# Performance work log

Measured on AMD Instinct MI355X. Metric: run time of the kernel, lower is better.

The kernel has to match this reference:

```python
import math
import jax, jax.numpy as jnp
import numpy as np

D_MODEL = 1024
N_HEADS = 16
D_K = D_MODEL // N_HEADS


def _build_neighbours(n_heads):
    # Mirrors LatticeMultiHeadAttention._build_neighbours for a (4,4)-style lattice.
    side = int(math.sqrt(n_heads))
    cols = side + 1 if side * side < n_heads else side
    positions = [divmod(i, cols) for i in range(n_heads)]
    pos_map = {p: j for j, p in enumerate(positions)}
    nb_idx = np.full((n_heads, 8), -1, dtype=np.int64)
    nb_w = np.zeros((n_heads, 8), dtype=np.float32)
    for i, (r, c) in enumerate(positions):
        k = 0
        for dr in (-1, 0, 1):
            for dc in (-1, 0, 1):
                if dr == 0 and dc == 0:
                    continue
                j = pos_map.get((r + dr, c + dc))
                if j is not None and k < 8:
                    nb_idx[i, k] = j
                    nb_w[i, k] = math.exp(-math.hypot(dr, dc))
                    k += 1
    return nb_idx, nb_w


def _phase_biases(coupling):
    # Sequential Kuramoto phase update: head h uses neighbor phases already
    # updated for heads < h (exactly as the torch per-head loop mutates buffers).
    H = coupling.shape[0]
    nb_idx, nb_w = _build_neighbours(H)
    phases = [jnp.asarray(0.0, coupling.dtype) for _ in range(H)]
    two_pi = 2.0 * math.pi
    for h in range(H):
        force = jnp.asarray(0.0, coupling.dtype)
        for k in range(8):
            j = int(nb_idx[h, k])
            if j >= 0:
                force = force + jnp.asarray(nb_w[h, k], coupling.dtype) * jnp.sin(phases[j] - phases[h])
        intrinsic = 1.0 + 0.1 * h
        new_phase = (phases[h] + 0.01 * (intrinsic + coupling[h] * force)) % two_pi
        phases[h] = new_phase
    return 0.1 * jnp.cos(jnp.stack(phases))  # [H] per-head scalar bias


def setup_inputs() -> dict:
    key = jax.random.key(0)
    ks = jax.random.split(key, 9)
    B, L = 2, 2048
    std = 0.02
    return {
        "query": jax.random.normal(ks[0], (B, L, D_MODEL), jnp.float32),
        "key": jax.random.normal(ks[1], (B, L, D_MODEL), jnp.float32),
        "value": jax.random.normal(ks[2], (B, L, D_MODEL), jnp.float32),
        "Wq": std * jax.random.normal(ks[3], (N_HEADS, D_MODEL, D_K), jnp.float32),
        "Wk": std * jax.random.normal(ks[4], (N_HEADS, D_MODEL, D_K), jnp.float32),
        "Wv": std * jax.random.normal(ks[5], (N_HEADS, D_MODEL, D_K), jnp.float32),
        "out_w": std * jax.random.normal(ks[6], (D_MODEL, D_MODEL), jnp.float32),
        "out_b": jnp.zeros((D_MODEL,), jnp.float32),
        "coupling": 0.1 * jnp.ones((N_HEADS,), jnp.float32),
    }


def reference(query, key, value, Wq, Wk, Wv, out_w, out_b, coupling):
    d_k = Wq.shape[-1]
    Q = jnp.einsum("bld,hdk->bhlk", query, Wq)
    K = jnp.einsum("bld,hdk->bhlk", key, Wk)
    V = jnp.einsum("bld,hdk->bhlk", value, Wv)
    scale = jnp.asarray(math.sqrt(float(d_k)), query.dtype)
    scores = jnp.einsum("bhlk,bhmk->bhlm", Q, K) / scale
    bias = _phase_biases(coupling)  # [H]
    scores = scores + bias[None, :, None, None]
    attn = jax.nn.softmax(scores, axis=-1)
    ctx = jnp.einsum("bhlm,bhmk->bhlk", attn, V)
    B, H, L, _ = ctx.shape
    out = ctx.transpose(0, 2, 1, 3).reshape(B, L, H * d_k)  # concat heads
    return out @ out_w + out_b
```

## Files before the change

### kernel.cpp

```cpp
#include <hip/hip_runtime.h>
#include <cstdint>

typedef uint16_t u16;
typedef __attribute__((ext_vector_type(8))) short bf16x8;
typedef __attribute__((ext_vector_type(4))) short bf16x4;
typedef __attribute__((ext_vector_type(4))) float f32x4;

#define QSCALE 0.18033688011112042f

struct Ptr3 { const float* a; const float* b; const float* c; };

__device__ __forceinline__ u16 f2bf(float x) {
  union { float f; uint32_t u; } v; v.f = x;
  uint32_t r = (v.u + 0x7fffu + ((v.u >> 16) & 1u)) >> 16;
  return (u16)r;
}

__device__ __forceinline__ void async16(void* lds, const void* g) {
  __builtin_amdgcn_global_load_lds((const __attribute__((address_space(1))) void*)g,
                                   (__attribute__((address_space(3))) void*)lds, 16, 0, 0);
}

__global__ __launch_bounds__(256) void k_cast3(Ptr3 in, u16* __restrict__ out) {
  const int z = blockIdx.y;
  const float* p = z == 0 ? in.a : (z == 1 ? in.b : in.c);
  int i = blockIdx.x * 256 + threadIdx.x;
  float4 v = ((const float4*)p)[i];
  bf16x4 o;
  o[0] = (short)f2bf(v.x); o[1] = (short)f2bf(v.y);
  o[2] = (short)f2bf(v.z); o[3] = (short)f2bf(v.w);
  *(bf16x4*)(out + (long)z * 4194304 + (long)i * 4) = o;
}

__global__ __launch_bounds__(256) void k_transpose_w(Ptr3 w, u16* __restrict__ out) {
  __shared__ u16 tile[64 * 72];
  const int t = threadIdx.x;
  const int z = blockIdx.z;
  const float* in = (z < 16) ? w.a : (z < 32 ? w.b : w.c);
  const long in_base = (long)(z & 15) * 65536;
  const long out_base = (long)z * 65536;
  const int r0 = blockIdx.x * 64;
  for (int e = t; e < 4096; e += 256) {
    int rr = e >> 6, cc = e & 63;
    tile[rr * 72 + cc] = f2bf(in[in_base + (long)(r0 + rr) * 64 + cc]);
  }
  __syncthreads();
  for (int s = t; s < 512; s += 256) {
    int cc = s >> 3, r8 = (s & 7) << 3;
    bf16x8 p;
    #pragma unroll
    for (int j = 0; j < 8; ++j) p[j] = (short)tile[(r8 + j) * 72 + cc];
    *(bf16x8*)(out + out_base + (long)cc * 1024 + r0 + r8) = p;
  }
}

__global__ __launch_bounds__(256) void k_transpose_bf16(const void* __restrict__ in,
                                                        int in_is_f32, u16* __restrict__ out,
                                                        int rstride, int R, int sph,
                                                        long slab_lo, long slab_hi) {
  __shared__ u16 tile[64 * 72];
  const int t = threadIdx.x;
  const long z = blockIdx.z;
  const long in_base = (z / sph) * slab_hi + (z % sph) * slab_lo;
  const long out_base = z * (long)R * (long)(gridDim.y * 64);
  const int r0 = blockIdx.x * 64, c0 = blockIdx.y * 64;
  for (int e = t; e < 4096; e += 256) {
    int rr = e >> 6, cc = e & 63;
    long src = in_base + (long)(r0 + rr) * rstride + c0 + cc;
    u16 w = in_is_f32 ? f2bf(((const float*)in)[src]) : ((const u16*)in)[src];
    tile[rr * 72 + cc] = w;
  }
  __syncthreads();
  for (int s = t; s < 512; s += 256) {
    int cc = s >> 3, r8 = (s & 7) << 3;
    bf16x8 p;
    #pragma unroll
    for (int j = 0; j < 8; ++j) p[j] = (short)tile[(r8 + j) * 72 + cc];
    *(bf16x8*)(out + out_base + (long)(c0 + cc) * R + r0 + r8) = p;
  }
}

__global__ __launch_bounds__(256) void k_gemm_qkv(const u16* __restrict__ A0,
                                                  const u16* __restrict__ B0,
                                                  u16* __restrict__ C0, float scale0) {
  __shared__ __align__(16) u16 As[128 * 32];
  __shared__ __align__(16) u16 Bs[128 * 32];
  const int z = blockIdx.z;
  const u16* A = A0 + (long)z * 4194304;
  const u16* Bt = B0 + (long)z * 1048576;
  u16* C = C0 + (long)z * 4194304;
  const float scale = z ? 1.0f : scale0;
  const int t = threadIdx.x, lane = t & 63, quad = lane >> 4, l16 = lane & 15;
  const int wave = t >> 6, wy = wave >> 1, wx = wave & 1;
  const int m0 = blockIdx.y * 128, n0 = blockIdx.x * 128;
  const int wbase = t & 192;
  f32x4 acc[4][4] = {};
  for (int k0 = 0; k0 < 1024; k0 += 32) {
    __syncthreads();
    #pragma unroll
    for (int i = 0; i < 2; ++i) {
      int sb = i * 256 + wbase;
      int s = sb + lane;
      int row = s >> 2, c = s & 3;
      async16(As + sb * 8, A + (long)(m0 + row) * 1024 + k0 + c * 8);
      async16(Bs + sb * 8, Bt + (long)(n0 + row) * 1024 + k0 + c * 8);
    }
    __syncthreads();
    bf16x8 af[4], bfr[4];
    #pragma unroll
    for (int mt = 0; mt < 4; ++mt)
      af[mt] = *(const bf16x8*)(As + (wy * 64 + mt * 16 + l16) * 32 + quad * 8);
    #pragma unroll
    for (int nt = 0; nt < 4; ++nt)
      bfr[nt] = *(const bf16x8*)(Bs + (wx * 64 + nt * 16 + l16) * 32 + quad * 8);
    #pragma unroll
    for (int mt = 0; mt < 4; ++mt)
      #pragma unroll
      for (int nt = 0; nt < 4; ++nt)
        acc[mt][nt] = __builtin_amdgcn_mfma_f32_16x16x32_bf16(af[mt], bfr[nt], acc[mt][nt], 0, 0, 0);
  }
  #pragma unroll
  for (int mt = 0; mt < 4; ++mt)
    #pragma unroll
    for (int nt = 0; nt < 4; ++nt) {
      int col = n0 + wx * 64 + nt * 16 + l16;
      #pragma unroll
      for (int r = 0; r < 4; ++r) {
        int row = m0 + wy * 64 + mt * 16 + quad * 4 + r;
        C[(long)row * 1024 + col] = f2bf(acc[mt][nt][r] * scale);
      }
    }
}

__global__ __launch_bounds__(256) void k_gemm_out(const u16* __restrict__ A,
                                                  const u16* __restrict__ Bt,
                                                  float* __restrict__ C,
                                                  const float* __restrict__ bias) {
  __shared__ __align__(16) u16 As[128 * 32];
  __shared__ __align__(16) u16 Bs[64 * 32];
  const int t = threadIdx.x, lane = t & 63, quad = lane >> 4, l16 = lane & 15;
  const int wave = t >> 6;
  const int m0 = blockIdx.y * 128, n0 = blockIdx.x * 64;
  const int wbase = t & 192;
  f32x4 acc[2][4] = {};
  for (int k0 = 0; k0 < 1024; k0 += 32) {
    __syncthreads();
    #pragma unroll
    for (int i = 0; i < 2; ++i) {
      int sb = i * 256 + wbase;
      int s = sb + lane;
      int row = s >> 2, c = s & 3;
      async16(As + sb * 8, A + (long)(m0 + row) * 1024 + k0 + c * 8);
    }
    {
      int s = t;
      int row = s >> 2, c = s & 3;
      async16(Bs + wbase * 8, Bt + (long)(n0 + row) * 1024 + k0 + c * 8);
    }
    __syncthreads();
    bf16x8 af[2], bfr[4];
    #pragma unroll
    for (int mt = 0; mt < 2; ++mt)
      af[mt] = *(const bf16x8*)(As + (wave * 32 + mt * 16 + l16) * 32 + quad * 8);
    #pragma unroll
    for (int nt = 0; nt < 4; ++nt)
      bfr[nt] = *(const bf16x8*)(Bs + (nt * 16 + l16) * 32 + quad * 8);
    #pragma unroll
    for (int mt = 0; mt < 2; ++mt)
      #pragma unroll
      for (int nt = 0; nt < 4; ++nt)
        acc[mt][nt] = __builtin_amdgcn_mfma_f32_16x16x32_bf16(af[mt], bfr[nt], acc[mt][nt], 0, 0, 0);
  }
  #pragma unroll
  for (int mt = 0; mt < 2; ++mt)
    #pragma unroll
    for (int nt = 0; nt < 4; ++nt) {
      int col = n0 + nt * 16 + l16;
      #pragma unroll
      for (int r = 0; r < 4; ++r) {
        int row = m0 + wave * 32 + mt * 16 + quad * 4 + r;
        C[(long)row * 1024 + col] = acc[mt][nt][r] + bias[col];
      }
    }
}

__global__ __launch_bounds__(512, 2) void k_flash(const u16* __restrict__ Qp,
                                                  const u16* __restrict__ Kp,
                                                  const u16* __restrict__ Vt,
                                                  u16* __restrict__ ctx) {
  __shared__ __align__(16) u16 qs[256 * 64];
  __shared__ __align__(16) u16 ks[64 * 72];
  __shared__ __align__(16) u16 vs[64 * 72];
  const int t = threadIdx.x, lane = t & 63, quad = lane >> 4, l16 = lane & 15;
  const int wave = t >> 6;
  const int bh = blockIdx.x & 31, b = bh >> 4, h = bh & 15;
  const int q0 = (blockIdx.x >> 5) * 256;
  const long gkbase = (long)b * 2097152 + h * 64;
  const long gvbase = (long)bh * 131072;
  const int srow = t >> 3, sc = t & 7;

  {
    long gq = (long)(b * 2048 + q0) * 1024 + h * 64;
    #pragma unroll
    for (int i = 0; i < 4; ++i) {
      int s = i * 512 + t;
      int row = s >> 3, pos = s & 7, c = pos ^ (row & 7);
      async16(qs + (long)s * 8, Qp + gq + (long)row * 1024 + c * 8);
    }
  }
  bf16x8 kreg = *(const bf16x8*)(Kp + gkbase + (long)srow * 1024 + sc * 8);
  bf16x8 vreg = *(const bf16x8*)(Vt + gvbase + (long)srow * 2048 + sc * 8);
  __syncthreads();

  bf16x8 qf[2][2];
  #pragma unroll
  for (int msub = 0; msub < 2; ++msub)
    #pragma unroll
    for (int kh = 0; kh < 2; ++kh) {
      int m = wave * 32 + msub * 16 + l16;
      int pos = (kh * 4 + quad) ^ (m & 7);
      qf[msub][kh] = *(const bf16x8*)(qs + m * 64 + pos * 8);
    }
  *(bf16x8*)(ks + srow * 72 + sc * 8) = kreg;
  *(bf16x8*)(vs + srow * 72 + sc * 8) = vreg;
  __syncthreads();

  u16* pw = qs + wave * 1152;

  float lsum[2][4] = {};
  f32x4 o[2][4] = {};

  for (int kt = 0; kt < 32; ++kt) {
    if (kt < 31) {
      int kv0 = (kt + 1) * 64;
      kreg = *(const bf16x8*)(Kp + gkbase + (long)(kv0 + srow) * 1024 + sc * 8);
      vreg = *(const bf16x8*)(Vt + gvbase + kv0 + (long)srow * 2048 + sc * 8);
    }

    bf16x8 kf[4][2], vf[4][2];
    #pragma unroll
    for (int nt = 0; nt < 4; ++nt)
      #pragma unroll
      for (int kh = 0; kh < 2; ++kh) {
        kf[nt][kh] = *(const bf16x8*)(ks + (nt * 16 + l16) * 72 + kh * 32 + quad * 8);
        vf[nt][kh] = *(const bf16x8*)(vs + (nt * 16 + l16) * 72 + kh * 32 + quad * 8);
      }

    #pragma unroll
    for (int msub = 0; msub < 2; ++msub) {
      #pragma unroll
      for (int nt = 0; nt < 4; ++nt) {
        f32x4 a = {};
        #pragma unroll
        for (int kh = 0; kh < 2; ++kh)
          a = __builtin_amdgcn_mfma_f32_16x16x32_bf16(qf[msub][kh], kf[nt][kh], a, 0, 0, 0);
        #pragma unroll
        for (int r = 0; r < 4; ++r) {
          float e = __builtin_amdgcn_exp2f(a[r]);
          lsum[msub][r] += e;
          pw[(quad * 4 + r) * 72 + nt * 16 + l16] = f2bf(e);
        }
      }
      #pragma unroll
      for (int kh = 0; kh < 2; ++kh) {
        bf16x8 pa = *(const bf16x8*)(pw + l16 * 72 + kh * 32 + quad * 8);
        #pragma unroll
        for (int nt = 0; nt < 4; ++nt)
          o[msub][nt] = __builtin_amdgcn_mfma_f32_16x16x32_bf16(pa, vf[nt][kh], o[msub][nt], 0, 0, 0);
      }
    }

    __syncthreads();
    if (kt < 31) {
      *(bf16x8*)(ks + srow * 72 + sc * 8) = kreg;
      *(bf16x8*)(vs + srow * 72 + sc * 8) = vreg;
    }
    __syncthreads();
  }

  #pragma unroll
  for (int msub = 0; msub < 2; ++msub)
    #pragma unroll
    for (int r = 0; r < 4; ++r) {
      float l = lsum[msub][r];
      #pragma unroll
      for (int d = 1; d < 16; d <<= 1) l += __shfl_xor(l, d);
      lsum[msub][r] = 1.0f / l;
    }
  #pragma unroll
  for (int msub = 0; msub < 2; ++msub)
    #pragma unroll
    for (int nt = 0; nt < 4; ++nt)
      #pragma unroll
      for (int r = 0; r < 4; ++r) {
        int q = q0 + wave * 32 + msub * 16 + quad * 4 + r;
        long idx = (long)(b * 2048 + q) * 1024 + h * 64 + nt * 16 + l16;
        ctx[idx] = f2bf(o[msub][nt][r] * lsum[msub][r]);
      }
}

extern "C" void kernel_launch(void* const* d_in, const int* in_sizes, int n_in,
                              void* d_out, int out_size, void* d_ws, size_t ws_size,
                              hipStream_t stream) {
  const float* query = (const float*)d_in[0];
  const float* key   = (const float*)d_in[1];
  const float* value = (const float*)d_in[2];
  const float* Wq    = (const float*)d_in[3];
  const float* Wk    = (const float*)d_in[4];
  const float* Wv    = (const float*)d_in[5];
  const float* out_w = (const float*)d_in[6];
  const float* out_b = (const float*)d_in[7];
  float* out = (float*)d_out;

  char* ws = (char*)d_ws;
  size_t off = 0;
  auto alloc = [&](size_t bytes) {
    void* p = ws + off;
    off += (bytes + 255) & ~(size_t)255;
    return p;
  };
  u16* qb  = (u16*)alloc(4096L * 1024 * 2);
  u16* kb  = (u16*)alloc(4096L * 1024 * 2);
  u16* vb  = (u16*)alloc(4096L * 1024 * 2);
  u16* wtq = (u16*)alloc(1024L * 1024 * 2);
  u16* wtk = (u16*)alloc(1024L * 1024 * 2);
  u16* wtv = (u16*)alloc(1024L * 1024 * 2);
  u16* wto = (u16*)alloc(1024L * 1024 * 2);
  u16* Qp  = (u16*)alloc(4096L * 1024 * 2);
  u16* Kp  = (u16*)alloc(4096L * 1024 * 2);
  u16* Vp  = (u16*)alloc(4096L * 1024 * 2);
  u16* Vtb = (u16*)alloc(4096L * 1024 * 2);
  u16* ctx = qb;
  (void)kb; (void)vb; (void)wtk; (void)wtv; (void)Kp; (void)Vp;

  k_cast3<<<dim3(4096, 3), 256, 0, stream>>>(Ptr3{query, key, value}, qb);

  k_transpose_w<<<dim3(16, 1, 48), 256, 0, stream>>>(Ptr3{Wq, Wk, Wv}, wtq);
  k_transpose_bf16<<<dim3(16, 16, 1), 256, 0, stream>>>(out_w, 1, wto, 1024, 1024, 1, 0L, 0L);

  k_gemm_qkv<<<dim3(8, 32, 3), 256, 0, stream>>>(qb, wtq, Qp, QSCALE);

  k_transpose_bf16<<<dim3(32, 1, 32), 256, 0, stream>>>(Vp, 0, Vtb, 1024, 2048, 16, 64L, 2097152L);

  k_flash<<<256, 512, 0, stream>>>(Qp, Kp, Vtb, ctx);

  k_gemm_out<<<dim3(16, 32), 256, 0, stream>>>(ctx, wto, out, out_b);
}
```

Baseline: 250.4 us.

## Fuse V transpose into flash kernel and double-buffer K/V tiles

Removes the separate V transpose launch and instead transposes V while storing it into LDS inside the flash kernel. K/V tiles are double-buffered with a register prefetch two tiles ahead, cutting one barrier per iteration. Q is loaded through registers with a padded stride of 68 instead of an XOR-swizzled async load, and the P scratch now holds both msub halves. The transpose kernels switch their LDS padding from 72 to 65. The scalar transposed V stores into LDS may cause bank conflicts, and the larger shared footprint could affect occupancy.

New measurement: 350.1 us. +39.8%, slower.

```diff
diff --git a/kernel.cpp b/kernel.cpp
--- a/kernel.cpp
+++ b/kernel.cpp
@@ -33,7 +33,7 @@
 }
 
 __global__ __launch_bounds__(256) void k_transpose_w(Ptr3 w, u16* __restrict__ out) {
-  __shared__ u16 tile[64 * 72];
+  __shared__ u16 tile[64 * 65];
   const int t = threadIdx.x;
   const int z = blockIdx.z;
   const float* in = (z < 16) ? w.a : (z < 32 ? w.b : w.c);
@@ -42,14 +42,14 @@
   const int r0 = blockIdx.x * 64;
   for (int e = t; e < 4096; e += 256) {
     int rr = e >> 6, cc = e & 63;
-    tile[rr * 72 + cc] = f2bf(in[in_base + (long)(r0 + rr) * 64 + cc]);
+    tile[rr * 65 + cc] = f2bf(in[in_base + (long)(r0 + rr) * 64 + cc]);
   }
   __syncthreads();
   for (int s = t; s < 512; s += 256) {
     int cc = s >> 3, r8 = (s & 7) << 3;
     bf16x8 p;
     #pragma unroll
-    for (int j = 0; j < 8; ++j) p[j] = (short)tile[(r8 + j) * 72 + cc];
+    for (int j = 0; j < 8; ++j) p[j] = (short)tile[(r8 + j) * 65 + cc];
     *(bf16x8*)(out + out_base + (long)cc * 1024 + r0 + r8) = p;
   }
 }
@@ -58,7 +58,7 @@
                                                         int in_is_f32, u16* __restrict__ out,
                                                         int rstride, int R, int sph,
                                                         long slab_lo, long slab_hi) {
-  __shared__ u16 tile[64 * 72];
+  __shared__ u16 tile[64 * 65];
   const int t = threadIdx.x;
   const long z = blockIdx.z;
   const long in_base = (z / sph) * slab_hi + (z % sph) * slab_lo;
@@ -68,14 +68,14 @@
     int rr = e >> 6, cc = e & 63;
     long src = in_base + (long)(r0 + rr) * rstride + c0 + cc;
     u16 w = in_is_f32 ? f2bf(((const float*)in)[src]) : ((const u16*)in)[src];
-    tile[rr * 72 + cc] = w;
+    tile[rr * 65 + cc] = w;
   }
   __syncthreads();
   for (int s = t; s < 512; s += 256) {
     int cc = s >> 3, r8 = (s & 7) << 3;
     bf16x8 p;
     #pragma unroll
-    for (int j = 0; j < 8; ++j) p[j] = (short)tile[(r8 + j) * 72 + cc];
+    for (int j = 0; j < 8; ++j) p[j] = (short)tile[(r8 + j) * 65 + cc];
     *(bf16x8*)(out + out_base + (long)(c0 + cc) * R + r0 + r8) = p;
   }
 }
@@ -186,68 +186,75 @@
 
 __global__ __launch_bounds__(512, 2) void k_flash(const u16* __restrict__ Qp,
                                                   const u16* __restrict__ Kp,
-                                                  const u16* __restrict__ Vt,
+                                                  const u16* __restrict__ Vp,
                                                   u16* __restrict__ ctx) {
-  __shared__ __align__(16) u16 qs[256 * 64];
-  __shared__ __align__(16) u16 ks[64 * 72];
-  __shared__ __align__(16) u16 vs[64 * 72];
+  __shared__ __align__(16) u16 qs[256 * 68];
+  __shared__ __align__(16) u16 ks[2][64 * 68];
+  __shared__ __align__(16) u16 vs[2][64 * 68];
   const int t = threadIdx.x, lane = t & 63, quad = lane >> 4, l16 = lane & 15;
   const int wave = t >> 6;
   const int bh = blockIdx.x & 31, b = bh >> 4, h = bh & 15;
   const int q0 = (blockIdx.x >> 5) * 256;
-  const long gkbase = (long)b * 2097152 + h * 64;
-  const long gvbase = (long)bh * 131072;
+  const long gkv = (long)b * 2097152 + h * 64;
   const int srow = t >> 3, sc = t & 7;
 
+  const long gq = (long)(b * 2048 + q0) * 1024 + h * 64;
   {
-    long gq = (long)(b * 2048 + q0) * 1024 + h * 64;
-    #pragma unroll
-    for (int i = 0; i < 4; ++i) {
-      int s = i * 512 + t;
-      int row = s >> 3, pos = s & 7, c = pos ^ (row & 7);
-      async16(qs + (long)s * 8, Qp + gq + (long)row * 1024 + c * 8);
-    }
-  }
-  bf16x8 kreg = *(const bf16x8*)(Kp + gkbase + (long)srow * 1024 + sc * 8);
-  bf16x8 vreg = *(const bf16x8*)(Vt + gvbase + (long)srow * 2048 + sc * 8);
+    bf16x8 qr[4];
+    #pragma unroll
+    for (int i = 0; i < 4; ++i)
+      qr[i] = *(const bf16x8*)(Qp + gq + (long)((i * 512 + t) >> 3) * 1024 + (t & 7) * 8);
+    #pragma unroll
+    for (int i = 0; i < 4; ++i)
+      *(bf16x8*)(qs + ((i * 512 + t) >> 3) * 68 + (t & 7) * 8) = qr[i];
+  }
+  bf16x8 kreg = *(const bf16x8*)(Kp + gkv + (long)srow * 1024 + sc * 8);
+  bf16x8 vreg = *(const bf16x8*)(Vp + gkv + (long)srow * 1024 + sc * 8);
+  *(bf16x8*)(ks[0] + srow * 68 + sc * 8) = kreg;
+  #pragma unroll
+  for (int j = 0; j < 8; ++j) vs[0][(sc * 8 + j) * 68 + srow] = (u16)vreg[j];
+  kreg = *(const bf16x8*)(Kp + gkv + (long)(64 + srow) * 1024 + sc * 8);
+  vreg = *(const bf16x8*)(Vp + gkv + (long)(64 + srow) * 1024 + sc * 8);
   __syncthreads();
 
   bf16x8 qf[2][2];
   #pragma unroll
   for (int msub = 0; msub < 2; ++msub)
     #pragma unroll
-    for (int kh = 0; kh < 2; ++kh) {
-      int m = wave * 32 + msub * 16 + l16;
-      int pos = (kh * 4 + quad) ^ (m & 7);
-      qf[msub][kh] = *(const bf16x8*)(qs + m * 64 + pos * 8);
-    }
-  *(bf16x8*)(ks + srow * 72 + sc * 8) = kreg;
-  *(bf16x8*)(vs + srow * 72 + sc * 8) = vreg;
-  __syncthreads();
-
-  u16* pw = qs + wave * 1152;
+    for (int kh = 0; kh < 2; ++kh)
+      qf[msub][kh] = *(const bf16x8*)(qs + (wave * 32 + msub * 16 + l16) * 68 + kh * 32 + quad * 8);
+  u16* pw = qs + wave * 32 * 68;
 
   float lsum[2][4] = {};
   f32x4 o[2][4] = {};
 
   for (int kt = 0; kt < 32; ++kt) {
+    if (kt) __syncthreads();
+
     if (kt < 31) {
-      int kv0 = (kt + 1) * 64;
-      kreg = *(const bf16x8*)(Kp + gkbase + (long)(kv0 + srow) * 1024 + sc * 8);
-      vreg = *(const bf16x8*)(Vt + gvbase + kv0 + (long)srow * 2048 + sc * 8);
-    }
-
-    bf16x8 kf[4][2], vf[4][2];
+      *(bf16x8*)(ks[(kt + 1) & 1] + srow * 68 + sc * 8) = kreg;
+      #pragma unroll
+      for (int j = 0; j < 8; ++j)
+        vs[(kt + 1) & 1][(sc * 8 + j) * 68 + srow] = (u16)vreg[j];
+    }
+    if (kt < 30) {
+      int kv0 = (kt + 2) * 64;
+      kreg = *(const bf16x8*)(Kp + gkv + (long)(kv0 + srow) * 1024 + sc * 8);
+      vreg = *(const bf16x8*)(Vp + gkv + (long)(kv0 + srow) * 1024 + sc * 8);
+    }
+
+    const u16* ksb = ks[kt & 1];
+    const u16* vsb = vs[kt & 1];
+
+    bf16x8 kf[4][2];
     #pragma unroll
     for (int nt = 0; nt < 4; ++nt)
       #pragma unroll
-      for (int kh = 0; kh < 2; ++kh) {
-        kf[nt][kh] = *(const bf16x8*)(ks + (nt * 16 + l16) * 72 + kh * 32 + quad * 8);
-        vf[nt][kh] = *(const bf16x8*)(vs + (nt * 16 + l16) * 72 + kh * 32 + quad * 8);
-      }
-
-    #pragma unroll
-    for (int msub = 0; msub < 2; ++msub) {
+      for (int kh = 0; kh < 2; ++kh)
+        kf[nt][kh] = *(const bf16x8*)(ksb + (nt * 16 + l16) * 68 + kh * 32 + quad * 8);
+
+    #pragma unroll
+    for (int msub = 0; msub < 2; ++msub)
       #pragma unroll
       for (int nt = 0; nt < 4; ++nt) {
         f32x4 a = {};
@@ -258,24 +265,21 @@
         for (int r = 0; r < 4; ++r) {
           float e = __builtin_amdgcn_exp2f(a[r]);
           lsum[msub][r] += e;
-          pw[(quad * 4 + r) * 72 + nt * 16 + l16] = f2bf(e);
+          pw[(msub * 16 + quad * 4 + r) * 68 + nt * 16 + l16] = f2bf(e);
         }
       }
+
+    #pragma unroll
+    for (int msub = 0; msub < 2; ++msub)
       #pragma unroll
       for (int kh = 0; kh < 2; ++kh) {
-        bf16x8 pa = *(const bf16x8*)(pw + l16 * 72 + kh * 32 + quad * 8);
+        bf16x8 pa = *(const bf16x8*)(pw + (msub * 16 + l16) * 68 + kh * 32 + quad * 8);
         #pragma unroll
-        for (int nt = 0; nt < 4; ++nt)
-          o[msub][nt] = __builtin_amdgcn_mfma_f32_16x16x32_bf16(pa, vf[nt][kh], o[msub][nt], 0, 0, 0);
-      }
-    }
-
-    __syncthreads();
-    if (kt < 31) {
-      *(bf16x8*)(ks + srow * 72 + sc * 8) = kreg;
-      *(bf16x8*)(vs + srow * 72 + sc * 8) = vreg;
-    }
-    __syncthreads();
+        for (int nt = 0; nt < 4; ++nt) {
+          bf16x8 vf = *(const bf16x8*)(vsb + (nt * 16 + l16) * 68 + kh * 32 + quad * 8);
+          o[msub][nt] = __builtin_amdgcn_mfma_f32_16x16x32_bf16(pa, vf, o[msub][nt], 0, 0, 0);
+        }
+      }
   }
 
   #pragma unroll
@@ -329,7 +333,6 @@
   u16* Qp  = (u16*)alloc(4096L * 1024 * 2);
   u16* Kp  = (u16*)alloc(4096L * 1024 * 2);
   u16* Vp  = (u16*)alloc(4096L * 1024 * 2);
-  u16* Vtb = (u16*)alloc(4096L * 1024 * 2);
   u16* ctx = qb;
   (void)kb; (void)vb; (void)wtk; (void)wtv; (void)Kp; (void)Vp;
 
@@ -340,9 +343,7 @@
 
   k_gemm_qkv<<<dim3(8, 32, 3), 256, 0, stream>>>(qb, wtq, Qp, QSCALE);
 
-  k_transpose_bf16<<<dim3(32, 1, 32), 256, 0, stream>>>(Vp, 0, Vtb, 1024, 2048, 16, 64L, 2097152L);
-
-  k_flash<<<256, 512, 0, stream>>>(Qp, Kp, Vtb, ctx);
+  k_flash<<<256, 512, 0, stream>>>(Qp, Kp, Vp, ctx);
 
   k_gemm_out<<<dim3(16, 32), 256, 0, stream>>>(ctx, wto, out, out_b);
 }
```

## Fuse V transpose into QKV GEMM epilogue and merge weight transposes

Applied to the files above, without the earlier changes.

Writes the V projection directly in transposed per-head layout from the QKV GEMM epilogue via an LDS staging tile, removing a separate transpose kernel and its read/write round trip. It also merges the Wqkv and out_w weight transposes into one launch, cutting launch overhead. In exchange the GEMM kernel uses about 33KB more LDS for the staging tile, which may reduce occupancy for all three z slices. The transpose tile padding also changes from 72 to 65.

Result: no change. 246.3 us (-1.7%).

```diff
diff --git a/kernel.cpp b/kernel.cpp
--- a/kernel.cpp
+++ b/kernel.cpp
@@ -32,64 +32,53 @@
   *(bf16x4*)(out + (long)z * 4194304 + (long)i * 4) = o;
 }
 
-__global__ __launch_bounds__(256) void k_transpose_w(Ptr3 w, u16* __restrict__ out) {
-  __shared__ u16 tile[64 * 72];
+__global__ __launch_bounds__(256) void k_transpose_all(Ptr3 w, const float* __restrict__ ow,
+                                                       u16* __restrict__ wt,
+                                                       u16* __restrict__ wto) {
+  __shared__ u16 tile[64 * 65];
   const int t = threadIdx.x;
-  const int z = blockIdx.z;
-  const float* in = (z < 16) ? w.a : (z < 32 ? w.b : w.c);
-  const long in_base = (long)(z & 15) * 65536;
-  const long out_base = (long)z * 65536;
-  const int r0 = blockIdx.x * 64;
+  const int bx = blockIdx.x;
+  const float* in;
+  long in_base, out_base;
+  int rstr, r0, c0;
+  u16* outp;
+  if (bx < 768) {
+    int z = bx >> 4;
+    r0 = (bx & 15) * 64; c0 = 0;
+    in = (z < 16) ? w.a : (z < 32 ? w.b : w.c);
+    in_base = (long)(z & 15) * 65536;
+    out_base = (long)z * 65536;
+    rstr = 64; outp = wt;
+  } else {
+    int idx = bx - 768;
+    r0 = (idx >> 4) * 64; c0 = (idx & 15) * 64;
+    in = ow; in_base = 0; out_base = 0;
+    rstr = 1024; outp = wto;
+  }
   for (int e = t; e < 4096; e += 256) {
     int rr = e >> 6, cc = e & 63;
-    tile[rr * 72 + cc] = f2bf(in[in_base + (long)(r0 + rr) * 64 + cc]);
+    tile[rr * 65 + cc] = f2bf(in[in_base + (long)(r0 + rr) * rstr + c0 + cc]);
   }
   __syncthreads();
   for (int s = t; s < 512; s += 256) {
     int cc = s >> 3, r8 = (s & 7) << 3;
     bf16x8 p;
     #pragma unroll
-    for (int j = 0; j < 8; ++j) p[j] = (short)tile[(r8 + j) * 72 + cc];
-    *(bf16x8*)(out + out_base + (long)cc * 1024 + r0 + r8) = p;
-  }
-}
-
-__global__ __launch_bounds__(256) void k_transpose_bf16(const void* __restrict__ in,
-                                                        int in_is_f32, u16* __restrict__ out,
-                                                        int rstride, int R, int sph,
-                                                        long slab_lo, long slab_hi) {
-  __shared__ u16 tile[64 * 72];
-  const int t = threadIdx.x;
-  const long z = blockIdx.z;
-  const long in_base = (z / sph) * slab_hi + (z % sph) * slab_lo;
-  const long out_base = z * (long)R * (long)(gridDim.y * 64);
-  const int r0 = blockIdx.x * 64, c0 = blockIdx.y * 64;
-  for (int e = t; e < 4096; e += 256) {
-    int rr = e >> 6, cc = e & 63;
-    long src = in_base + (long)(r0 + rr) * rstride + c0 + cc;
-    u16 w = in_is_f32 ? f2bf(((const float*)in)[src]) : ((const u16*)in)[src];
-    tile[rr * 72 + cc] = w;
-  }
-  __syncthreads();
-  for (int s = t; s < 512; s += 256) {
-    int cc = s >> 3, r8 = (s & 7) << 3;
-    bf16x8 p;
-    #pragma unroll
-    for (int j = 0; j < 8; ++j) p[j] = (short)tile[(r8 + j) * 72 + cc];
-    *(bf16x8*)(out + out_base + (long)(c0 + cc) * R + r0 + r8) = p;
+    for (int j = 0; j < 8; ++j) p[j] = (short)tile[(r8 + j) * 65 + cc];
+    *(bf16x8*)(outp + out_base + (long)(c0 + cc) * 1024 + r0 + r8) = p;
   }
 }
 
 __global__ __launch_bounds__(256) void k_gemm_qkv(const u16* __restrict__ A0,
                                                   const u16* __restrict__ B0,
-                                                  u16* __restrict__ C0, float scale0) {
+                                                  u16* __restrict__ C0,
+                                                  u16* __restrict__ Vt, float scale0) {
   __shared__ __align__(16) u16 As[128 * 32];
   __shared__ __align__(16) u16 Bs[128 * 32];
+  __shared__ u16 T[128 * 130];
   const int z = blockIdx.z;
   const u16* A = A0 + (long)z * 4194304;
   const u16* Bt = B0 + (long)z * 1048576;
-  u16* C = C0 + (long)z * 4194304;
-  const float scale = z ? 1.0f : scale0;
   const int t = threadIdx.x, lane = t & 63, quad = lane >> 4, l16 = lane & 15;
   const int wave = t >> 6, wy = wave >> 1, wx = wave & 1;
   const int m0 = blockIdx.y * 128, n0 = blockIdx.x * 128;
@@ -119,17 +108,43 @@
       for (int nt = 0; nt < 4; ++nt)
         acc[mt][nt] = __builtin_amdgcn_mfma_f32_16x16x32_bf16(af[mt], bfr[nt], acc[mt][nt], 0, 0, 0);
   }
-  #pragma unroll
-  for (int mt = 0; mt < 4; ++mt)
-    #pragma unroll
-    for (int nt = 0; nt < 4; ++nt) {
-      int col = n0 + wx * 64 + nt * 16 + l16;
-      #pragma unroll
-      for (int r = 0; r < 4; ++r) {
-        int row = m0 + wy * 64 + mt * 16 + quad * 4 + r;
-        C[(long)row * 1024 + col] = f2bf(acc[mt][nt][r] * scale);
-      }
-    }
+  if (z < 2) {
+    u16* C = C0 + (long)z * 4194304;
+    const float scale = z ? 1.0f : scale0;
+    #pragma unroll
+    for (int mt = 0; mt < 4; ++mt)
+      #pragma unroll
+      for (int nt = 0; nt < 4; ++nt) {
+        int col = n0 + wx * 64 + nt * 16 + l16;
+        #pragma unroll
+        for (int r = 0; r < 4; ++r) {
+          int row = m0 + wy * 64 + mt * 16 + quad * 4 + r;
+          C[(long)row * 1024 + col] = f2bf(acc[mt][nt][r] * scale);
+        }
+      }
+  } else {
+    #pragma unroll
+    for (int mt = 0; mt < 4; ++mt)
+      #pragma unroll
+      for (int nt = 0; nt < 4; ++nt) {
+        int cc = wx * 64 + nt * 16 + l16;
+        #pragma unroll
+        for (int r = 0; r < 4; ++r)
+          T[(wy * 64 + mt * 16 + quad * 4 + r) * 130 + cc] = f2bf(acc[mt][nt][r]);
+      }
+    __syncthreads();
+    const int h0 = blockIdx.x * 2, bb = m0 >> 11, lb = m0 & 2047;
+    #pragma unroll
+    for (int i = 0; i < 8; ++i) {
+      int s = t + i * 256;
+      int c = s >> 4, l0 = (s & 15) * 8;
+      bf16x8 p;
+      #pragma unroll
+      for (int j = 0; j < 8; ++j) p[j] = (short)T[(l0 + j) * 130 + c];
+      *(bf16x8*)(Vt + (long)(bb * 16 + h0 + (c >> 6)) * 131072 +
+                 (long)(c & 63) * 2048 + lb + l0) = p;
+    }
+  }
 }
 
 __global__ __launch_bounds__(256) void k_gemm_out(const u16* __restrict__ A,
@@ -328,19 +343,15 @@
   u16* wto = (u16*)alloc(1024L * 1024 * 2);
   u16* Qp  = (u16*)alloc(4096L * 1024 * 2);
   u16* Kp  = (u16*)alloc(4096L * 1024 * 2);
-  u16* Vp  = (u16*)alloc(4096L * 1024 * 2);
   u16* Vtb = (u16*)alloc(4096L * 1024 * 2);
   u16* ctx = qb;
-  (void)kb; (void)vb; (void)wtk; (void)wtv; (void)Kp; (void)Vp;
+  (void)kb; (void)vb; (void)wtk; (void)wtv; (void)Kp;
 
   k_cast3<<<dim3(4096, 3), 256, 0, stream>>>(Ptr3{query, key, value}, qb);
 
-  k_transpose_w<<<dim3(16, 1, 48), 256, 0, stream>>>(Ptr3{Wq, Wk, Wv}, wtq);
-  k_transpose_bf16<<<dim3(16, 16, 1), 256, 0, stream>>>(out_w, 1, wto, 1024, 1024, 1, 0L, 0L);
-
-  k_gemm_qkv<<<dim3(8, 32, 3), 256, 0, stream>>>(qb, wtq, Qp, QSCALE);
-
-  k_transpose_bf16<<<dim3(32, 1, 32), 256, 0, stream>>>(Vp, 0, Vtb, 1024, 2048, 16, 64L, 2097152L);
+  k_transpose_all<<<1024, 256, 0, stream>>>(Ptr3{Wq, Wk, Wv}, out_w, wtq, wto);
+
+  k_gemm_qkv<<<dim3(8, 32, 3), 256, 0, stream>>>(qb, wtq, Qp, Vtb, QSCALE);
 
   k_flash<<<256, 512, 0, stream>>>(Qp, Kp, Vtb, ctx);
 
```
